# Kernel tuning notes

Measured on AMD Instinct MI355X. Metric: run time of the kernel, lower is better.

The kernel has to match this reference:

```python
import jax, jax.numpy as jnp
import numpy as np
from jax import lax

C = 32           # cell_state_size (channels, depthwise groups)
B = 4            # batch
D = H = W = 64   # lattice dims
STEPS = 8        # propagation depth


def setup_inputs() -> dict:
    key = jax.random.key(0)
    k1, k2 = jax.random.split(key)
    cube_states = jax.random.normal(k1, (B, C, D, H, W), dtype=jnp.float32)
    # torch depthwise Conv3d weight: [C_out, C_in/groups=1, 3, 3, 3]
    weight = jax.random.normal(k2, (C, 1, 3, 3, 3), dtype=jnp.float32) * 0.1
    return {"cube_states": cube_states, "weight": weight, "depth": STEPS}


def _depthwise_conv3d(x, w):
    # x: [B, C, D, H, W], w: [C, 1, 3, 3, 3] -> depthwise via feature_group_count=C
    return lax.conv_general_dilated(
        x, w,
        window_strides=(1, 1, 1),
        padding=((1, 1), (1, 1), (1, 1)),
        dimension_numbers=("NCDHW", "OIDHW", "NCDHW"),
        feature_group_count=C,
    )


def reference(cube_states, weight, depth):
    x = cube_states
    for _ in range(depth):
        residual = _depthwise_conv3d(x, weight)
        x = jax.nn.gelu(x + residual, approximate=False)  # torch nn.GELU() is exact (erf)
    return x
```

## Files before the change

### kernel.cpp

```cpp
#include <hip/hip_runtime.h>
#include <math.h>

#define Bn 4
#define Cn 32
#define Dn 64
#define Hn 64
#define Wn 64
#define PLANE (Hn * Wn)
#define DT 16
#define LSTRIDE 68
#define LROWS 66
#define LPLANE (LROWS * LSTRIDE)

__device__ __forceinline__ float gelu_exact(float x) {
    float s = fabsf(x) * 0.70710678118654752f;
    float t = __builtin_amdgcn_rcpf(fmaf(0.3275911f, s, 1.0f));
    float P = t * fmaf(t, fmaf(t, fmaf(t, fmaf(t, 1.061405429f, -1.453152027f),
                                       1.421413741f), -0.284496736f), 0.254829592f);
    float E = __builtin_amdgcn_exp2f(-s * s * 1.4426950408889634f);
    float q = P * E;
    float hxq = 0.5f * x * q;
    return x > 0.f ? x - hxq : hxq;
}

__device__ __forceinline__ void read_row(const float* base, float f[10]) {
    float4 a = *(const float4*)(base);
    float4 b = *(const float4*)(base + 4);
    float2 c = *(const float2*)(base + 8);
    f[0] = a.x; f[1] = a.y; f[2] = a.z; f[3] = a.w;
    f[4] = b.x; f[5] = b.y; f[6] = b.z; f[7] = b.w;
    f[8] = c.x; f[9] = c.y;
}

__device__ __forceinline__ void acc_row(const float f[10], float w0t, float w1t,
                                        float w2t, float acc[8]) {
#pragma unroll
    for (int j = 0; j < 8; j++) {
        acc[j] = fmaf(f[j],     w0t, acc[j]);
        acc[j] = fmaf(f[j + 1], w1t, acc[j]);
        acc[j] = fmaf(f[j + 2], w2t, acc[j]);
    }
}

__global__ __launch_bounds__(512, 4)
void EmergentSpatialPropagation_step(const float* __restrict__ src,
                                     const float* __restrict__ wgt,
                                     float* __restrict__ dst) {
    __shared__ float lds[4 * LPLANE];

    const int tid = threadIdx.x;
    const int d0  = blockIdx.x * DT;
    const int c   = blockIdx.y;
    const int b   = blockIdx.z;
    const size_t base = ((size_t)(b * Cn + c)) * (size_t)(Dn * PLANE);

    for (int i = tid; i < 4 * LPLANE; i += 512) lds[i] = 0.0f;

    float wt[27];
#pragma unroll
    for (int k = 0; k < 27; k++) wt[k] = wgt[c * 27 + k];

    const int h  = tid >> 3;
    const int w0 = (tid & 7) << 3;
    const int m  = tid & 15;

    auto slot = [&](int p) -> float* { return &lds[((p + 1) & 3) * LPLANE]; };

    auto load_g = [&](int p, float4 G[2]) {
        if ((unsigned)p < (unsigned)Dn) {
            const float4* g = (const float4*)(src + base + (size_t)p * PLANE);
            G[0] = g[tid];
            G[1] = g[512 + tid];
        } else {
            G[0] = make_float4(0.f, 0.f, 0.f, 0.f);
            G[1] = make_float4(0.f, 0.f, 0.f, 0.f);
        }
    };

    auto write_plane = [&](int p, const float4 G[2]) {
        float* pl = slot(p);
#pragma unroll
        for (int i = 0; i < 2; i++) {
            int idx = i * 512 + tid;
            int row = (idx >> 4) + 1;
            float prev = __shfl_up(G[i].w, 1);
            if (m == 0) prev = 0.f;
            float4 W = make_float4(prev, G[i].x, G[i].y, G[i].z);
            *(float4*)(pl + row * LSTRIDE + 4 * m) = W;
            if (m == 15) pl[row * LSTRIDE + 64] = G[i].w;
        }
    };

    __syncthreads();
    {
        float4 Ga[2], Gb[2], Gc[2];
        load_g(d0 - 1, Ga); load_g(d0, Gb); load_g(d0 + 1, Gc);
        write_plane(d0 - 1, Ga); write_plane(d0, Gb); write_plane(d0 + 1, Gc);
    }
    __syncthreads();

    float C0[3][10], C1[3][10];
#pragma unroll
    for (int ky = 0; ky < 3; ky++)
        read_row(slot(d0) + (h + ky) * LSTRIDE + w0, C0[ky]);

    for (int it = 0; it < DT; it++) {
        const int dz = d0 + it;

        float4 G[2];
        if (it < DT - 1) load_g(dz + 2, G);

#pragma unroll
        for (int ky = 0; ky < 3; ky++)
            read_row(slot(dz + 1) + (h + ky) * LSTRIDE + w0, C1[ky]);

        float acc[8] = {0, 0, 0, 0, 0, 0, 0, 0};

#pragma unroll
        for (int ky = 0; ky < 3; ky++) {
            float T[10];
            read_row(slot(dz - 1) + (h + ky) * LSTRIDE + w0, T);
            acc_row(T, wt[ky * 3 + 0], wt[ky * 3 + 1], wt[ky * 3 + 2], acc);
        }
#pragma unroll
        for (int ky = 0; ky < 3; ky++)
            acc_row(C0[ky], wt[9 + ky * 3 + 0], wt[9 + ky * 3 + 1], wt[9 + ky * 3 + 2], acc);
#pragma unroll
        for (int ky = 0; ky < 3; ky++)
            acc_row(C1[ky], wt[18 + ky * 3 + 0], wt[18 + ky * 3 + 1], wt[18 + ky * 3 + 2], acc);

        float* dptr = dst + base + (size_t)dz * PLANE + h * Wn + w0;
#pragma unroll
        for (int j = 0; j < 8; j++)
            dptr[j] = gelu_exact(C0[1][j + 1] + acc[j]);

        if (it < DT - 1) {
            write_plane(dz + 2, G);
            __syncthreads();
        }

#pragma unroll
        for (int ky = 0; ky < 3; ky++)
#pragma unroll
            for (int k = 0; k < 10; k++) C0[ky][k] = C1[ky][k];
    }
}

extern "C" void kernel_launch(void* const* d_in, const int* in_sizes, int n_in,
                              void* d_out, int out_size, void* d_ws, size_t ws_size,
                              hipStream_t stream) {
    const float* x   = (const float*)d_in[0];
    const float* wgt = (const float*)d_in[1];
    float* out = (float*)d_out;
    float* ws  = (float*)d_ws;

    dim3 grid(Dn / DT, Cn, Bn);
    dim3 block(512);

    const float* src = x;
    for (int s = 0; s < 8; s++) {
        float* dst = (s & 1) ? out : ws;
        EmergentSpatialPropagation_step<<<grid, block, 0, stream>>>(src, wgt, dst);
        src = dst;
    }
}
```

Measured before the change: 749.8 us.

## Keep three depth planes in a register ring and halve the LDS buffer

Each step now keeps the previous, current and next depth-plane neighbourhoods in three rotating register arrays, so the dz-1 plane is no longer re-read from LDS. The loop is unrolled by three so the rotation needs no copies. Because of this, LDS drops from four plane slots to two, which should allow more resident blocks per CU. The thread-to-(h,w) mapping is reshuffled and outputs are written as float4 vector stores. The cost is about 90 floats of live plane data per thread under the 512-thread, 4-wave launch bound, which risks register spills.

Measured after the change: 1.595 ms. +112.7%, slower.

```diff
diff --git a/kernel.cpp b/kernel.cpp
--- a/kernel.cpp
+++ b/kernel.cpp
@@ -46,7 +46,7 @@
 void EmergentSpatialPropagation_step(const float* __restrict__ src,
                                      const float* __restrict__ wgt,
                                      float* __restrict__ dst) {
-    __shared__ float lds[4 * LPLANE];
+    __shared__ __align__(16) float lds[2 * LPLANE];
 
     const int tid = threadIdx.x;
     const int d0  = blockIdx.x * DT;
@@ -54,17 +54,17 @@
     const int b   = blockIdx.z;
     const size_t base = ((size_t)(b * Cn + c)) * (size_t)(Dn * PLANE);
 
-    for (int i = tid; i < 4 * LPLANE; i += 512) lds[i] = 0.0f;
+    for (int i = tid; i < 2 * LPLANE; i += 512) lds[i] = 0.0f;
 
     float wt[27];
 #pragma unroll
     for (int k = 0; k < 27; k++) wt[k] = wgt[c * 27 + k];
 
-    const int h  = tid >> 3;
-    const int w0 = (tid & 7) << 3;
+    const int h  = (tid & 7) | ((tid >> 6) << 3);
+    const int w0 = ((tid >> 3) & 7) << 3;
     const int m  = tid & 15;
 
-    auto slot = [&](int p) -> float* { return &lds[((p + 1) & 3) * LPLANE]; };
+    auto sl = [&](int p) -> float* { return &lds[((p - d0 + 1) & 1) * LPLANE]; };
 
     auto load_g = [&](int p, float4 G[2]) {
         if ((unsigned)p < (unsigned)Dn) {
@@ -77,73 +77,91 @@
         }
     };
 
-    auto write_plane = [&](int p, const float4 G[2]) {
-        float* pl = slot(p);
+    auto write_plane = [&](float* pl, const float4 G[2]) {
 #pragma unroll
         for (int i = 0; i < 2; i++) {
             int idx = i * 512 + tid;
             int row = (idx >> 4) + 1;
             float prev = __shfl_up(G[i].w, 1);
             if (m == 0) prev = 0.f;
-            float4 W = make_float4(prev, G[i].x, G[i].y, G[i].z);
-            *(float4*)(pl + row * LSTRIDE + 4 * m) = W;
+            float4 Wv = make_float4(prev, G[i].x, G[i].y, G[i].z);
+            *(float4*)(pl + row * LSTRIDE + 4 * m) = Wv;
             if (m == 15) pl[row * LSTRIDE + 64] = G[i].w;
         }
     };
 
+    auto read3 = [&](const float* pl, float (&P)[3][10]) {
+#pragma unroll
+        for (int ky = 0; ky < 3; ky++)
+            read_row(pl + (h + ky) * LSTRIDE + w0, P[ky]);
+    };
+
+    float PA[3][10], PB[3][10], PC[3][10];
+
     __syncthreads();
     {
-        float4 Ga[2], Gb[2], Gc[2];
-        load_g(d0 - 1, Ga); load_g(d0, Gb); load_g(d0 + 1, Gc);
-        write_plane(d0 - 1, Ga); write_plane(d0, Gb); write_plane(d0 + 1, Gc);
+        float4 Ga[2], Gb[2];
+        load_g(d0 - 1, Ga); load_g(d0, Gb);
+        write_plane(sl(d0 - 1), Ga); write_plane(sl(d0), Gb);
+    }
+    __syncthreads();
+    read3(sl(d0 - 1), PA);
+    read3(sl(d0),     PB);
+    {
+        float4 Gc[2];
+        load_g(d0 + 1, Gc);
+        __syncthreads();
+        write_plane(sl(d0 + 1), Gc);
     }
     __syncthreads();
 
-    float C0[3][10], C1[3][10];
-#pragma unroll
-    for (int ky = 0; ky < 3; ky++)
-        read_row(slot(d0) + (h + ky) * LSTRIDE + w0, C0[ky]);
-
-    for (int it = 0; it < DT; it++) {
+    auto body = [&](int it, bool last, float (&Pm1)[3][10], float (&P0)[3][10],
+                    float (&P1)[3][10]) {
         const int dz = d0 + it;
 
         float4 G[2];
-        if (it < DT - 1) load_g(dz + 2, G);
+        if (!last) load_g(dz + 2, G);
 
+        read3(sl(dz + 1), P1);
+
+        float acc[8];
+#pragma unroll
+        for (int j = 0; j < 8; j++) acc[j] = 0.f;
 #pragma unroll
         for (int ky = 0; ky < 3; ky++)
-            read_row(slot(dz + 1) + (h + ky) * LSTRIDE + w0, C1[ky]);
-
-        float acc[8] = {0, 0, 0, 0, 0, 0, 0, 0};
-
-#pragma unroll
-        for (int ky = 0; ky < 3; ky++) {
-            float T[10];
-            read_row(slot(dz - 1) + (h + ky) * LSTRIDE + w0, T);
-            acc_row(T, wt[ky * 3 + 0], wt[ky * 3 + 1], wt[ky * 3 + 2], acc);
-        }
+            acc_row(Pm1[ky], wt[ky * 3 + 0], wt[ky * 3 + 1], wt[ky * 3 + 2], acc);
 #pragma unroll
         for (int ky = 0; ky < 3; ky++)
-            acc_row(C0[ky], wt[9 + ky * 3 + 0], wt[9 + ky * 3 + 1], wt[9 + ky * 3 + 2], acc);
+            acc_row(P0[ky], wt[9 + ky * 3 + 0], wt[9 + ky * 3 + 1], wt[9 + ky * 3 + 2], acc);
 #pragma unroll
         for (int ky = 0; ky < 3; ky++)
-            acc_row(C1[ky], wt[18 + ky * 3 + 0], wt[18 + ky * 3 + 1], wt[18 + ky * 3 + 2], acc);
+            acc_row(P1[ky], wt[18 + ky * 3 + 0], wt[18 + ky * 3 + 1], wt[18 + ky * 3 + 2], acc);
 
         float* dptr = dst + base + (size_t)dz * PLANE + h * Wn + w0;
-#pragma unroll
-        for (int j = 0; j < 8; j++)
-            dptr[j] = gelu_exact(C0[1][j + 1] + acc[j]);
+        float4 o0 = make_float4(gelu_exact(P0[1][1] + acc[0]),
+                                gelu_exact(P0[1][2] + acc[1]),
+                                gelu_exact(P0[1][3] + acc[2]),
+                                gelu_exact(P0[1][4] + acc[3]));
+        float4 o1 = make_float4(gelu_exact(P0[1][5] + acc[4]),
+                                gelu_exact(P0[1][6] + acc[5]),
+                                gelu_exact(P0[1][7] + acc[6]),
+                                gelu_exact(P0[1][8] + acc[7]));
+        *(float4*)(dptr)     = o0;
+        *(float4*)(dptr + 4) = o1;
 
-        if (it < DT - 1) {
-            write_plane(dz + 2, G);
+        if (!last) {
+            write_plane(sl(dz + 2), G);
             __syncthreads();
         }
+    };
 
-#pragma unroll
-        for (int ky = 0; ky < 3; ky++)
-#pragma unroll
-            for (int k = 0; k < 10; k++) C0[ky][k] = C1[ky][k];
+#pragma unroll 1
+    for (int bs = 0; bs < DT - 1; bs += 3) {
+        body(bs + 0, false, PA, PB, PC);
+        body(bs + 1, false, PB, PC, PA);
+        body(bs + 2, false, PC, PA, PB);
     }
+    body(DT - 1, true, PA, PB, PC);
 }
 
 extern "C" void kernel_launch(void* const* d_in, const int* in_sizes, int n_in,
```

## Replace LDS staging with direct global row loads and wave shuffles for halos

Applied to the files above, without the earlier changes.

The shared-memory ring of padded planes and its per-plane barriers are removed. Each thread now loads its own three rows (h-1, h, h+1) straight from global memory and builds the W-halo with cross-lane shuffles. Each loaded plane is scattered into three rotating output accumulators, one per depth tap, so every input plane is read once per thread. This drops the LDS traffic and __syncthreads, but triples global/L2 row reads per plane and loses the prefetch overlap the old loop had.

After: 962.3 us. +28.3%, slower.

```diff
diff --git a/kernel.cpp b/kernel.cpp
--- a/kernel.cpp
+++ b/kernel.cpp
@@ -8,9 +8,6 @@
 #define Wn 64
 #define PLANE (Hn * Wn)
 #define DT 16
-#define LSTRIDE 68
-#define LROWS 66
-#define LPLANE (LROWS * LSTRIDE)
 
 __device__ __forceinline__ float gelu_exact(float x) {
     float s = fabsf(x) * 0.70710678118654752f;
@@ -21,15 +18,6 @@
     float q = P * E;
     float hxq = 0.5f * x * q;
     return x > 0.f ? x - hxq : hxq;
-}
-
-__device__ __forceinline__ void read_row(const float* base, float f[10]) {
-    float4 a = *(const float4*)(base);
-    float4 b = *(const float4*)(base + 4);
-    float2 c = *(const float2*)(base + 8);
-    f[0] = a.x; f[1] = a.y; f[2] = a.z; f[3] = a.w;
-    f[4] = b.x; f[5] = b.y; f[6] = b.z; f[7] = b.w;
-    f[8] = c.x; f[9] = c.y;
 }
 
 __device__ __forceinline__ void acc_row(const float f[10], float w0t, float w1t,
@@ -46,15 +34,11 @@
 void EmergentSpatialPropagation_step(const float* __restrict__ src,
                                      const float* __restrict__ wgt,
                                      float* __restrict__ dst) {
-    __shared__ float lds[4 * LPLANE];
-
     const int tid = threadIdx.x;
     const int d0  = blockIdx.x * DT;
     const int c   = blockIdx.y;
     const int b   = blockIdx.z;
     const size_t base = ((size_t)(b * Cn + c)) * (size_t)(Dn * PLANE);
-
-    for (int i = tid; i < 4 * LPLANE; i += 512) lds[i] = 0.0f;
 
     float wt[27];
 #pragma unroll
@@ -62,88 +46,99 @@
 
     const int h  = tid >> 3;
     const int w0 = (tid & 7) << 3;
-    const int m  = tid & 15;
+    const int lw = tid & 7;
 
-    auto slot = [&](int p) -> float* { return &lds[((p + 1) & 3) * LPLANE]; };
+    const int hm = (h == 0) ? 0 : h - 1;
+    const int hp = (h == Hn - 1) ? Hn - 1 : h + 1;
+    const bool has_m = (h > 0);
+    const bool has_p = (h < Hn - 1);
 
-    auto load_g = [&](int p, float4 G[2]) {
-        if ((unsigned)p < (unsigned)Dn) {
-            const float4* g = (const float4*)(src + base + (size_t)p * PLANE);
-            G[0] = g[tid];
-            G[1] = g[512 + tid];
-        } else {
-            G[0] = make_float4(0.f, 0.f, 0.f, 0.f);
-            G[1] = make_float4(0.f, 0.f, 0.f, 0.f);
-        }
-    };
+    const int offm = hm * Wn + w0;
+    const int offc = h  * Wn + w0;
+    const int offp = hp * Wn + w0;
 
-    auto write_plane = [&](int p, const float4 G[2]) {
-        float* pl = slot(p);
+    const float4 z4 = make_float4(0.f, 0.f, 0.f, 0.f);
+
+    float A0[8], A1[8], A2[8];
 #pragma unroll
-        for (int i = 0; i < 2; i++) {
-            int idx = i * 512 + tid;
-            int row = (idx >> 4) + 1;
-            float prev = __shfl_up(G[i].w, 1);
-            if (m == 0) prev = 0.f;
-            float4 W = make_float4(prev, G[i].x, G[i].y, G[i].z);
-            *(float4*)(pl + row * LSTRIDE + 4 * m) = W;
-            if (m == 15) pl[row * LSTRIDE + 64] = G[i].w;
-        }
-    };
+    for (int j = 0; j < 8; j++) { A0[j] = 0.f; A1[j] = 0.f; A2[j] = 0.f; }
 
-    __syncthreads();
-    {
-        float4 Ga[2], Gb[2], Gc[2];
-        load_g(d0 - 1, Ga); load_g(d0, Gb); load_g(d0 + 1, Gc);
-        write_plane(d0 - 1, Ga); write_plane(d0, Gb); write_plane(d0 + 1, Gc);
+    float4 pcx0 = z4, pcx1 = z4;
+
+#define ROW_WIN(F, R0v, R1v)                          \
+    {                                                 \
+        float el = __shfl_up((R1v).w, 1);             \
+        float er = __shfl_down((R0v).x, 1);           \
+        F[0] = (lw == 0) ? 0.f : el;                  \
+        F[1] = (R0v).x; F[2] = (R0v).y;               \
+        F[3] = (R0v).z; F[4] = (R0v).w;               \
+        F[5] = (R1v).x; F[6] = (R1v).y;               \
+        F[7] = (R1v).z; F[8] = (R1v).w;               \
+        F[9] = (lw == 7) ? 0.f : er;                  \
     }
-    __syncthreads();
 
-    float C0[3][10], C1[3][10];
-#pragma unroll
-    for (int ky = 0; ky < 3; ky++)
-        read_row(slot(d0) + (h + ky) * LSTRIDE + w0, C0[ky]);
+#define BODY(JJ, AL, AM, AH, DOL, DOM, DOH)                                    \
+    do {                                                                       \
+        const int p = d0 - 1 + (JJ);                                           \
+        float4 m0, m1, c0, c1, q0, q1;                                         \
+        if ((unsigned)p < (unsigned)Dn) {                                      \
+            const float* g = src + base + (size_t)p * PLANE;                   \
+            m0 = *(const float4*)(g + offm); m1 = *(const float4*)(g + offm + 4); \
+            c0 = *(const float4*)(g + offc); c1 = *(const float4*)(g + offc + 4); \
+            q0 = *(const float4*)(g + offp); q1 = *(const float4*)(g + offp + 4); \
+            if (!has_m) { m0 = z4; m1 = z4; }                                  \
+            if (!has_p) { q0 = z4; q1 = z4; }                                  \
+        } else {                                                               \
+            m0 = z4; m1 = z4; c0 = z4; c1 = z4; q0 = z4; q1 = z4;              \
+        }                                                                      \
+        float fm[10], fc[10], fq[10];                                          \
+        ROW_WIN(fm, m0, m1); ROW_WIN(fc, c0, c1); ROW_WIN(fq, q0, q1);         \
+        if (DOH) {                        \
+            acc_row(fm, wt[0], wt[1], wt[2], AH);                              \
+            acc_row(fc, wt[3], wt[4], wt[5], AH);                              \
+            acc_row(fq, wt[6], wt[7], wt[8], AH);                              \
+        }                                                                      \
+        if (DOM) {                        \
+            acc_row(fm, wt[9],  wt[10], wt[11], AM);                           \
+            acc_row(fc, wt[12], wt[13], wt[14], AM);                           \
+            acc_row(fq, wt[15], wt[16], wt[17], AM);                           \
+        }                                                                      \
+        if (DOL) {                        \
+            acc_row(fm, wt[18], wt[19], wt[20], AL);                           \
+            acc_row(fc, wt[21], wt[22], wt[23], AL);                           \
+            acc_row(fq, wt[24], wt[25], wt[26], AL);                           \
+            float* dp = dst + base + (size_t)(p - 1) * PLANE + offc;           \
+            float4 o0 = make_float4(gelu_exact(pcx0.x + AL[0]),                \
+                                    gelu_exact(pcx0.y + AL[1]),                \
+                                    gelu_exact(pcx0.z + AL[2]),                \
+                                    gelu_exact(pcx0.w + AL[3]));               \
+            float4 o1 = make_float4(gelu_exact(pcx1.x + AL[4]),                \
+                                    gelu_exact(pcx1.y + AL[5]),                \
+                                    gelu_exact(pcx1.z + AL[6]),                \
+                                    gelu_exact(pcx1.w + AL[7]));               \
+            *(float4*)(dp)     = o0;      \
+            *(float4*)(dp + 4) = o1;                                           \
+        }                                                                      \
+        _Pragma("unroll")                                                      \
+        for (int j = 0; j < 8; j++) AL[j] = 0.f;          \
+        pcx0 = c0; pcx1 = c1;                                                  \
+    } while (0)
 
-    for (int it = 0; it < DT; it++) {
-        const int dz = d0 + it;
+    BODY(0, A0, A1, A2, 0, 0, 1);
+    BODY(1, A1, A2, A0, 0, 1, 1);
+    BODY(2, A2, A0, A1, 1, 1, 1);
+#pragma unroll 1
+    for (int u = 3; u < 15; u += 3) {
+        BODY(u,     A0, A1, A2, 1, 1, 1);
+        BODY(u + 1, A1, A2, A0, 1, 1, 1);
+        BODY(u + 2, A2, A0, A1, 1, 1, 1);
+    }
+    BODY(15, A0, A1, A2, 1, 1, 1);
+    BODY(16, A1, A2, A0, 1, 1, 0);
+    BODY(17, A2, A0, A1, 1, 0, 0);
 
-        float4 G[2];
-        if (it < DT - 1) load_g(dz + 2, G);
-
-#pragma unroll
-        for (int ky = 0; ky < 3; ky++)
-            read_row(slot(dz + 1) + (h + ky) * LSTRIDE + w0, C1[ky]);
-
-        float acc[8] = {0, 0, 0, 0, 0, 0, 0, 0};
-
-#pragma unroll
-        for (int ky = 0; ky < 3; ky++) {
-            float T[10];
-            read_row(slot(dz - 1) + (h + ky) * LSTRIDE + w0, T);
-            acc_row(T, wt[ky * 3 + 0], wt[ky * 3 + 1], wt[ky * 3 + 2], acc);
-        }
-#pragma unroll
-        for (int ky = 0; ky < 3; ky++)
-            acc_row(C0[ky], wt[9 + ky * 3 + 0], wt[9 + ky * 3 + 1], wt[9 + ky * 3 + 2], acc);
-#pragma unroll
-        for (int ky = 0; ky < 3; ky++)
-            acc_row(C1[ky], wt[18 + ky * 3 + 0], wt[18 + ky * 3 + 1], wt[18 + ky * 3 + 2], acc);
-
-        float* dptr = dst + base + (size_t)dz * PLANE + h * Wn + w0;
-#pragma unroll
-        for (int j = 0; j < 8; j++)
-            dptr[j] = gelu_exact(C0[1][j + 1] + acc[j]);
-
-        if (it < DT - 1) {
-            write_plane(dz + 2, G);
-            __syncthreads();
-        }
-
-#pragma unroll
-        for (int ky = 0; ky < 3; ky++)
-#pragma unroll
-            for (int k = 0; k < 10; k++) C0[ky][k] = C1[ky][k];
-    }
+#undef BODY
+#undef ROW_WIN
 }
 
 extern "C" void kernel_launch(void* const* d_in, const int* in_sizes, int n_in,
```
